# Optimization experiments

Hardware: AMD Instinct MI355X
Metric: run time of the kernel (lower is better)

## Reference

```python
import jax, jax.numpy as jnp
import numpy as np

B, S, H, V = 64, 256, 512, 512


def setup_inputs() -> dict:
    key = jax.random.key(0)
    ks = jax.random.split(key, 13)
    s = 1.0 / np.sqrt(H)
    f = jnp.float32
    return {
        "encoder_outputs": jax.random.normal(ks[0], (B, S, H), f),
        "Wa": jax.random.normal(ks[1], (H, H), f) * s,
        "ba": jax.random.normal(ks[2], (H,), f) * s,
        "Ua": jax.random.normal(ks[3], (H, H), f) * s,
        "bu": jax.random.normal(ks[4], (H,), f) * s,
        "Va": jax.random.normal(ks[5], (1, H), f) * s,
        "bv": jax.random.normal(ks[6], (1,), f) * s,
        "W_ih": jax.random.normal(ks[7], (3 * H, H), f) * s,
        "b_ih": jax.random.normal(ks[8], (3 * H,), f) * s,
        "W_hh": jax.random.normal(ks[9], (3 * H, H), f) * s,
        "b_hh": jax.random.normal(ks[10], (3 * H,), f) * s,
        "Wout": jax.random.normal(ks[11], (V, H), f) * s,
        "bout": jax.random.normal(ks[12], (V,), f) * s,
    }


def reference(encoder_outputs, Wa, ba, Ua, bu, Va, bv,
              W_ih, b_ih, W_hh, b_hh, Wout, bout):
    b, seq_len, h_dim = encoder_outputs.shape
    # Ua(keys) is loop-invariant: precompute once. [B,S,H]
    keys_proj = jnp.einsum('bsh,kh->bsk', encoder_outputs, Ua) + bu
    va = Va[0]  # [H]

    def step(h, _):
        # Bahdanau attention: query = current hidden [B,H]
        q = h @ Wa.T + ba                                   # [B,H]
        e = jnp.tanh(q[:, None, :] + keys_proj)             # [B,S,H]
        scores = jnp.einsum('bsh,h->bs', e, va) + bv[0]     # [B,S]
        w = jax.nn.softmax(scores, axis=-1)                 # [B,S]
        ctx = jnp.einsum('bs,bsh->bh', w, encoder_outputs)  # [B,H]
        # GRU cell (PyTorch gate order: r, z, n)
        gi = ctx @ W_ih.T + b_ih                            # [B,3H]
        gh = h @ W_hh.T + b_hh                              # [B,3H]
        gi_r, gi_z, gi_n = jnp.split(gi, 3, axis=-1)
        gh_r, gh_z, gh_n = jnp.split(gh, 3, axis=-1)
        r = jax.nn.sigmoid(gi_r + gh_r)
        z = jax.nn.sigmoid(gi_z + gh_z)
        n = jnp.tanh(gi_n + r * gh_n)
        h_new = (1.0 - z) * n + z * h                       # [B,H]
        logits = h_new @ Wout.T + bout                      # [B,V]
        return h_new, (logits, w)

    h0 = jnp.zeros((b, h_dim), encoder_outputs.dtype)
    h_final, (logits, ws) = jax.lax.scan(step, h0, None, length=seq_len)
    log_probs = jax.nn.log_softmax(logits, axis=-1)         # [S,B,V]
    attentions = jnp.transpose(ws, (1, 0, 2))               # [B,S,S]
    return log_probs, h_final[None], attentions
```

## Files before the change

### kernel.cpp

```cpp
#include <hip/hip_runtime.h>


typedef short s8v __attribute__((ext_vector_type(8)));
typedef float f4v __attribute__((ext_vector_type(4)));
typedef float f2v __attribute__((ext_vector_type(2)));

#define OFF_BAR   0u
#define OFF_H     2048u
#define OFF_HBF   133120u
#define OFF_Q     198656u
#define OFF_GH    329728u
#define OFF_CTX   722944u
#define OFF_ZP    854016u
#define OFF_WEXP  855040u
#define OFF_WCAT  920576u
#define OFF_WIH   3542016u
#define OFF_UAB   5114880u
#define OFF_KEYS  5639168u
#define OFF_ENC8  22416384u
#define WS_FULL   30804992u
#define MEMSET_BYTES 198656u

#define OUT_LOGITS 0u
#define OUT_HFIN   8388608u
#define OUT_ATTN   8421376u

__device__ __forceinline__ unsigned short f2bf(float f) {
  union { float f; unsigned u; } a; a.f = f;
  unsigned r = a.u + 0x7fffu + ((a.u >> 16) & 1u);
  return (unsigned short)(r >> 16);
}
__device__ __forceinline__ float bfbits2f(unsigned bits) {
  union { unsigned u; float f; } a; a.u = bits; return a.f;
}
__device__ __forceinline__ float bf2f(unsigned short h) { return bfbits2f((unsigned)h << 16); }

__device__ __forceinline__ float cload(const float* p) {
  return __hip_atomic_load(p, __ATOMIC_RELAXED, __HIP_MEMORY_SCOPE_AGENT);
}
__device__ __forceinline__ void cstore(float* p, float v) {
  __hip_atomic_store(p, v, __ATOMIC_RELAXED, __HIP_MEMORY_SCOPE_AGENT);
}
__device__ __forceinline__ unsigned long long cload64(const unsigned long long* p) {
  return __hip_atomic_load(p, __ATOMIC_RELAXED, __HIP_MEMORY_SCOPE_AGENT);
}
__device__ __forceinline__ void cstore64(unsigned long long* p, unsigned long long v) {
  __hip_atomic_store(p, v, __ATOMIC_RELAXED, __HIP_MEMORY_SCOPE_AGENT);
}
__device__ __forceinline__ unsigned long long pack2f(float a, float b) {
  union { float f[2]; unsigned long long u; } x; x.f[0] = a; x.f[1] = b; return x.u;
}

__device__ __forceinline__ float sigm(float x) {
  return __builtin_amdgcn_rcpf(1.f + __expf(-x));
}
__device__ __forceinline__ float tanh2(float x) {
  return 1.f - 2.f * __builtin_amdgcn_rcpf(1.f + __expf(x + x));
}
__device__ __forceinline__ f4v mfma16(s8v a, s8v b, f4v c) {
  return __builtin_amdgcn_mfma_f32_16x16x32_bf16(a, b, c, 0, 0, 0);
}

__device__ __forceinline__ void gbar(unsigned* bar, unsigned& gen) {
  asm volatile("s_waitcnt vmcnt(0) lgkmcnt(0)" ::: "memory");
  __syncthreads();
  if (threadIdx.x == 0) {
    __atomic_signal_fence(__ATOMIC_SEQ_CST);
    gen++;
    const int leaf = blockIdx.x >> 5;
    unsigned old = __hip_atomic_fetch_add(bar + 16 + leaf * 16, 1u, __ATOMIC_RELAXED,
                                          __HIP_MEMORY_SCOPE_AGENT);
    if (old == gen * 32u - 1u) {
      unsigned ro = __hip_atomic_fetch_add(bar, 1u, __ATOMIC_RELAXED,
                                           __HIP_MEMORY_SCOPE_AGENT);
      if (ro == gen * 8u - 1u) {
#pragma unroll
        for (int l = 0; l < 8; ++l)
          __hip_atomic_store(bar + 160 + l * 16, gen, __ATOMIC_RELAXED,
                             __HIP_MEMORY_SCOPE_AGENT);
      }
    }
    while (__hip_atomic_load(bar + 160 + leaf * 16, __ATOMIC_RELAXED,
                             __HIP_MEMORY_SCOPE_AGENT) < gen)
      __builtin_amdgcn_s_sleep(1);
    __atomic_signal_fence(__ATOMIC_SEQ_CST);
  }
  __syncthreads();
}

__global__ void __launch_bounds__(256) prep_kernel(
    const float* __restrict__ Wa, const float* __restrict__ Whh,
    const float* __restrict__ Wout, const float* __restrict__ Wih,
    const float* __restrict__ Ua, const float* __restrict__ enc,
    unsigned short* __restrict__ wcat, unsigned short* __restrict__ wihb,
    unsigned short* __restrict__ uab, unsigned char* __restrict__ enc8,
    int use_enc8) {
  const size_t gid = (size_t)blockIdx.x * 256 + threadIdx.x;
  const size_t stride = (size_t)gridDim.x * 256;
  for (size_t i = gid; i < 2359296u; i += stride) {
    float v; unsigned short* d;
    if (i < 1310720u) {
      v = (i < 262144u) ? Wa[i] : (i < 1048576u) ? Whh[i - 262144u] : Wout[i - 1048576u];
      d = wcat + i;
    } else if (i < 2097152u) { v = Wih[i - 1310720u]; d = wihb + (i - 1310720u); }
    else                     { v = Ua[i - 2097152u];  d = uab  + (i - 2097152u); }
    *d = f2bf(v);
  }
  if (use_enc8) {
    for (size_t j = gid; j < 4194304u; j += stride) {
      float2 e = ((const float2*)enc)[j];
      int pk = __builtin_amdgcn_cvt_pk_fp8_f32(e.x, e.y, 0, false);
      ((unsigned short*)enc8)[j] = (unsigned short)(pk & 0xffff);
    }
  }
}

__global__ void __launch_bounds__(256) keys_kernel(
    const float* __restrict__ enc, const unsigned short* __restrict__ uab,
    const float* __restrict__ bu, unsigned short* __restrict__ keysb) {
  const int tid = threadIdx.x;
  const int w = tid >> 6, lane = tid & 63, ln = lane & 15, kq = lane >> 4;
  const int mb = blockIdx.x >> 3, nb = blockIdx.x & 7;
  const int mrow = mb * 64 + w * 16 + ln;
  f4v acc[4] = {{0,0,0,0},{0,0,0,0},{0,0,0,0},{0,0,0,0}};
  for (int ks = 0; ks < 16; ++ks) {
    const float* ap = enc + (size_t)mrow * 512 + ks * 32 + kq * 8;
    s8v af;
#pragma unroll
    for (int j = 0; j < 8; ++j) af[j] = (short)f2bf(ap[j]);
#pragma unroll
    for (int nt = 0; nt < 4; ++nt) {
      int n = nb * 64 + nt * 16 + ln;
      s8v bf = ((const s8v*)(uab + (size_t)n * 512))[ks * 4 + kq];
      acc[nt] = mfma16(af, bf, acc[nt]);
    }
  }
#pragma unroll
  for (int nt = 0; nt < 4; ++nt) {
    int n = nb * 64 + nt * 16 + ln;
    float bias = bu[n];
#pragma unroll
    for (int r = 0; r < 4; ++r) {
      int gm = mb * 64 + w * 16 + kq * 4 + r;
      keysb[(size_t)gm * 512 + n] = f2bf(__expf(2.f * (acc[nt][r] + bias)));
    }
  }
}

__global__ void __launch_bounds__(256, 1) decoder_kernel(
    const float* __restrict__ enc, const float* __restrict__ ba_,
    const float* __restrict__ va_, const float* __restrict__ bih_,
    const float* __restrict__ bhh_, const float* __restrict__ bout_,
    const unsigned short* __restrict__ wcat, const unsigned short* __restrict__ wih,
    const unsigned short* __restrict__ keysb, const unsigned char* __restrict__ enc8,
    unsigned* __restrict__ bar, float* __restrict__ hst,
    unsigned short* __restrict__ hbf, float* __restrict__ qst,
    float* __restrict__ ghst, float* __restrict__ ctxst,
    float* __restrict__ zpst, float* __restrict__ wexpst,
    float* __restrict__ out, int use_enc8) {
  const int bid = blockIdx.x, tid = threadIdx.x;
  const int w = tid >> 6, lane = tid & 63, ln = lane & 15, kq = lane >> 4;
  __shared__ float s_w[64];
  unsigned gen = 0;
  float* logits = out + OUT_LOGITS;
  float* hfin = out + OUT_HFIN;
  float* attn = out + OUT_ATTN;

  const int pb_b = (bid & 7) * 8 + ((bid >> 3) >> 2);
  const int pb_p = (bid >> 3) & 3;
  float vav[8]; float vasum = 0.f;
#pragma unroll
  for (int j = 0; j < 8; ++j) { vav[j] = va_[lane * 8 + j]; vasum += vav[j]; }
#pragma unroll
  for (int off = 32; off > 0; off >>= 1) vasum += __shfl_xor(vasum, off, 64);

#pragma clang loop unroll(disable)
  for (int it = 0; it <= 256; ++it) {
    if (bid < 160) {
      const int C0 = bid * 16;
      const int rg = (C0 < 512) ? 0 : (C0 < 2048) ? 1 : 2;
      if (!((rg == 2 && it == 0) || (rg != 2 && it == 256))) {
        const s8v* wp = (const s8v*)(wcat + (size_t)(C0 + ln) * 512);
        const unsigned long long* hb =
            (const unsigned long long*)(hbf + (size_t)(w * 16 + ln) * 512);
        unsigned long long t[32];
#pragma unroll
        for (int ks = 0; ks < 16; ++ks) {
          t[2 * ks]     = cload64(hb + ks * 8 + kq * 2);
          t[2 * ks + 1] = cload64(hb + ks * 8 + kq * 2 + 1);
        }
        f4v acc = {0.f, 0.f, 0.f, 0.f};
#pragma unroll
        for (int ks = 0; ks < 16; ++ks) {
          union { unsigned long long u[2]; s8v v; } au;
          au.u[0] = t[2 * ks]; au.u[1] = t[2 * ks + 1];
          acc = mfma16(au.v, wp[ks * 4 + kq], acc);
        }
        const int col = C0 + ln;
        float bias = (rg == 0) ? ba_[col] : (rg == 1) ? bhh_[col - 512] : bout_[col - 2048];
#pragma unroll
        for (int r = 0; r < 4; ++r) {
          int b = w * 16 + kq * 4 + r;
          float v = acc[r] + bias;
          if (rg == 0)      cstore(qst + (size_t)b * 512 + col, v);
          else if (rg == 1) cstore(ghst + (size_t)b * 1536 + (col - 512), v);
          else if (it > 0)
            cstore(logits + (size_t)(it - 1) * 32768 + (size_t)b * 512 + (col - 2048), v);
        }
      }
    } else if (bid < 224 && it < 256) {
      int i = (bid - 160) * 512 + tid;
      cstore(ctxst + i, 0.f);
      cstore(ctxst + i + 256, 0.f);
    }
    gbar(bar, gen);
    if (it == 256) break;

    {
      const unsigned long long* q64 =
          (const unsigned long long*)(qst + (size_t)pb_b * 512 + lane * 8);
      unsigned long long tq[4];
#pragma unroll
      for (int j = 0; j < 4; ++j) tq[j] = cload64(q64 + j);
      union { unsigned long long u[4]; float f[8]; } qu;
#pragma unroll
      for (int j = 0; j < 4; ++j) qu.u[j] = tq[j];
      float Eq[8];
#pragma unroll
      for (int j = 0; j < 8; ++j) Eq[j] = __expf(2.f * qu.f[j]);
#pragma unroll 4
      for (int i = 0; i < 16; ++i) {
        const int sl = w * 16 + i;
        const s8v kv =
            ((const s8v*)(keysb + (size_t)(pb_b * 256 + pb_p * 64 + sl) * 512))[lane];
        float a2 = 0.f;
#pragma unroll
        for (int j = 0; j < 8; ++j) {
          float P = Eq[j] * bf2f((unsigned short)kv[j]);
          a2 += vav[j] * __builtin_amdgcn_rcpf(1.f + P);
        }
#pragma unroll
        for (int off = 32; off > 0; off >>= 1) a2 += __shfl_xor(a2, off, 64);
        if (lane == 0) s_w[sl] = __expf(vasum - 2.f * a2);
      }
      __syncthreads();
      float c0 = 0.f, c1 = 0.f;
      if (use_enc8) {
        const unsigned char* ep = enc8 + (size_t)(pb_b * 256 + pb_p * 64) * 512 + tid * 2;
#pragma unroll 8
        for (int s = 0; s < 64; ++s) {
          float wt = s_w[s];
          unsigned short e8 = *(const unsigned short*)(ep + (size_t)s * 512);
          f2v ef = __builtin_amdgcn_cvt_pk_f32_fp8((int)e8, false);
          c0 += wt * ef[0];
          c1 += wt * ef[1];
        }
      } else {
#pragma unroll 8
        for (int s = 0; s < 64; ++s) {
          float wt = s_w[s];
          float2 e = ((const float2*)(enc + (size_t)(pb_b * 256 + pb_p * 64 + s) * 512))[tid];
          c0 += wt * e.x; c1 += wt * e.y;
        }
      }
      atomicAdd(ctxst + (size_t)pb_b * 512 + tid * 2, c0);
      atomicAdd(ctxst + (size_t)pb_b * 512 + tid * 2 + 1, c1);
      if (tid < 64) {
        float z = s_w[tid];
        cstore(wexpst + (size_t)pb_b * 256 + pb_p * 64 + tid, z);
#pragma unroll
        for (int off = 32; off > 0; off >>= 1) z += __shfl_xor(z, off, 64);
        if (tid == 0) cstore(zpst + pb_b * 4 + pb_p, z);
      }
    }
    gbar(bar, gen);

    if (bid < 32) {
      const int b = w * 16 + ln;
      const unsigned long long* zp64 = (const unsigned long long*)(zpst + b * 4);
      const unsigned long long* cx = (const unsigned long long*)(ctxst + (size_t)b * 512);
      unsigned long long tz0 = cload64(zp64), tz1 = cload64(zp64 + 1);
      unsigned long long t[32];
#pragma unroll
      for (int ks = 0; ks < 8; ++ks)
#pragma unroll
        for (int u = 0; u < 4; ++u)
          t[ks * 4 + u] = cload64(cx + ks * 16 + kq * 4 + u);
      union { unsigned long long u; float f[2]; } z0, z1;
      z0.u = tz0; z1.u = tz1;
      float Z = z0.f[0] + z0.f[1] + z1.f[0] + z1.f[1];
      float invZ = __builtin_amdgcn_rcpf(Z);
      unsigned long long t2[32];
#pragma unroll
      for (int ks = 0; ks < 8; ++ks)
#pragma unroll
        for (int u = 0; u < 4; ++u)
          t2[ks * 4 + u] = cload64(cx + (ks + 8) * 16 + kq * 4 + u);
      f4v ar = {0,0,0,0}, az = {0,0,0,0}, an = {0,0,0,0};
      const s8v* wr = (const s8v*)(wih + (size_t)(bid * 16 + ln) * 512);
      const s8v* wz = (const s8v*)(wih + (size_t)(512 + bid * 16 + ln) * 512);
      const s8v* wn = (const s8v*)(wih + (size_t)(1024 + bid * 16 + ln) * 512);
#pragma unroll
      for (int ks = 0; ks < 16; ++ks) {
        union { unsigned long long u[4]; float f[8]; } cu;
#pragma unroll
        for (int u = 0; u < 4; ++u)
          cu.u[u] = (ks < 8) ? t[ks * 4 + u] : t2[(ks - 8) * 4 + u];
        s8v bfv;
#pragma unroll
        for (int j = 0; j < 8; ++j) bfv[j] = (short)f2bf(cu.f[j] * invZ);
        int idx = ks * 4 + kq;
        ar = mfma16(wr[idx], bfv, ar);
        az = mfma16(wz[idx], bfv, az);
        an = mfma16(wn[idx], bfv, an);
      }
      const int c0i = bid * 16 + kq * 4;
      const int cq = c0i >> 1;
      const unsigned long long* gh64 = (const unsigned long long*)(ghst + (size_t)b * 1536);
      const unsigned long long* h64  = (const unsigned long long*)(hst + (size_t)b * 512);
      unsigned long long tg[8];
      tg[0] = cload64(gh64 + cq);       tg[1] = cload64(gh64 + cq + 1);
      tg[2] = cload64(gh64 + 256 + cq); tg[3] = cload64(gh64 + 256 + cq + 1);
      tg[4] = cload64(gh64 + 512 + cq); tg[5] = cload64(gh64 + 512 + cq + 1);
      tg[6] = cload64(h64 + cq);        tg[7] = cload64(h64 + cq + 1);
      union { unsigned long long u[2]; float f[4]; } gr, gz, gn, hh;
      gr.u[0] = tg[0]; gr.u[1] = tg[1];
      gz.u[0] = tg[2]; gz.u[1] = tg[3];
      gn.u[0] = tg[4]; gn.u[1] = tg[5];
      hh.u[0] = tg[6]; hh.u[1] = tg[7];
      float hn[4]; unsigned short h4[4];
#pragma unroll
      for (int r = 0; r < 4; ++r) {
        int c = c0i + r;
        float rg2 = sigm(ar[r] + bih_[c] + gr.f[r]);
        float zg = sigm(az[r] + bih_[512 + c] + gz.f[r]);
        float ng = tanh2(an[r] + bih_[1024 + c] + rg2 * gn.f[r]);
        hn[r] = (1.f - zg) * ng + zg * hh.f[r];
        h4[r] = f2bf(hn[r]);
      }
      cstore64((unsigned long long*)(hst + (size_t)b * 512 + c0i), pack2f(hn[0], hn[1]));
      cstore64((unsigned long long*)(hst + (size_t)b * 512 + c0i + 2), pack2f(hn[2], hn[3]));
      union { unsigned short s[4]; unsigned long long u; } hb4;
      hb4.s[0] = h4[0]; hb4.s[1] = h4[1]; hb4.s[2] = h4[2]; hb4.s[3] = h4[3];
      cstore64((unsigned long long*)(hbf + (size_t)b * 512 + c0i), hb4.u);
    } else if (bid < 96) {
      const int b = bid - 32;
      unsigned long long tz0 = cload64((const unsigned long long*)(zpst + b * 4));
      unsigned long long tz1 = cload64((const unsigned long long*)(zpst + b * 4) + 1);
      float we = cload(wexpst + (size_t)b * 256 + tid);
      union { unsigned long long u; float f[2]; } z0, z1;
      z0.u = tz0; z1.u = tz1;
      float Z = z0.f[0] + z0.f[1] + z1.f[0] + z1.f[1];
      attn[(size_t)b * 65536 + (size_t)it * 256 + tid] = we * __builtin_amdgcn_rcpf(Z);
    }
    gbar(bar, gen);
  }

  for (int rit = 0; rit < 16; ++rit) {
    int row = bid * 64 + rit * 4 + w;
    float* xr = logits + (size_t)row * 512;
    f4v a = ((const f4v*)xr)[lane * 2];
    f4v b2 = ((const f4v*)xr)[lane * 2 + 1];
    float m = a[0];
#pragma unroll
    for (int j = 1; j < 4; ++j) m = fmaxf(m, a[j]);
#pragma unroll
    for (int j = 0; j < 4; ++j) m = fmaxf(m, b2[j]);
#pragma unroll
    for (int off = 32; off > 0; off >>= 1) m = fmaxf(m, __shfl_xor(m, off, 64));
    float sm = 0.f;
#pragma unroll
    for (int j = 0; j < 4; ++j) sm += __expf(a[j] - m) + __expf(b2[j] - m);
#pragma unroll
    for (int off = 32; off > 0; off >>= 1) sm += __shfl_xor(sm, off, 64);
    float lse = m + __logf(sm);
    f4v oa, ob;
#pragma unroll
    for (int j = 0; j < 4; ++j) { oa[j] = a[j] - lse; ob[j] = b2[j] - lse; }
    ((f4v*)xr)[lane * 2] = oa;
    ((f4v*)xr)[lane * 2 + 1] = ob;
  }
  {
    int i = bid * 256 + tid;
    if (i < 32768) hfin[i] = cload(hst + i);
  }
}

extern "C" void kernel_launch(void* const* d_in, const int* in_sizes, int n_in,
                              void* d_out, int out_size, void* d_ws, size_t ws_size,
                              hipStream_t stream) {
  const float* enc  = (const float*)d_in[0];
  const float* Wa   = (const float*)d_in[1];
  const float* ba   = (const float*)d_in[2];
  const float* Ua   = (const float*)d_in[3];
  const float* bu   = (const float*)d_in[4];
  const float* Va   = (const float*)d_in[5];
  const float* Wih  = (const float*)d_in[7];
  const float* bih  = (const float*)d_in[8];
  const float* Whh  = (const float*)d_in[9];
  const float* bhh  = (const float*)d_in[10];
  const float* Wout = (const float*)d_in[11];
  const float* bout = (const float*)d_in[12];
  (void)in_sizes; (void)n_in; (void)out_size;

  char* ws = (char*)d_ws;
  unsigned*       bar   = (unsigned*)(ws + OFF_BAR);
  float*          hst   = (float*)(ws + OFF_H);
  unsigned short* hbf   = (unsigned short*)(ws + OFF_HBF);
  float*          qst   = (float*)(ws + OFF_Q);
  float*          ghst  = (float*)(ws + OFF_GH);
  float*          ctxst = (float*)(ws + OFF_CTX);
  float*          zpst  = (float*)(ws + OFF_ZP);
  float*          wexp  = (float*)(ws + OFF_WEXP);
  unsigned short* wcat  = (unsigned short*)(ws + OFF_WCAT);
  unsigned short* wihb  = (unsigned short*)(ws + OFF_WIH);
  unsigned short* uab   = (unsigned short*)(ws + OFF_UAB);
  unsigned short* keysb = (unsigned short*)(ws + OFF_KEYS);
  unsigned char*  enc8  = (unsigned char*)(ws + OFF_ENC8);
  int use_enc8 = (ws_size >= (size_t)WS_FULL) ? 1 : 0;

  hipMemsetAsync(d_ws, 0, MEMSET_BYTES, stream);
  prep_kernel<<<1024, 256, 0, stream>>>(Wa, Whh, Wout, Wih, Ua, enc,
                                        wcat, wihb, uab, enc8, use_enc8);
  keys_kernel<<<2048, 256, 0, stream>>>(enc, uab, bu, keysb);
  decoder_kernel<<<256, 256, 0, stream>>>(enc, ba, Va, bih, bhh, bout,
                                          wcat, wihb, keysb, enc8,
                                          bar, hst, hbf, qst, ghst, ctxst,
                                          zpst, wexp, (float*)d_out, use_enc8);
}
```

Baseline: 10.10 ms.

## Restructure decoder into 64 batch-owning blocks with flat barrier and transposed keys

Rewrites the persistent decoder so each of 64 blocks of 512 threads owns one batch row. Attention scores, softmax and the context are computed entirely within that block, using a transposed keys layout and shared-memory reductions, which replaces cross-block atomic context accumulation. The two-level tree barrier becomes a single-counter barrier over 64 blocks. GRU and output projections are redistributed, with the gh and logits partials accumulated in zeroed workspace and output buffers, and the bout bias is folded into the final log-softmax. The output buffer now needs an extra memset. Fewer blocks means less parallelism per step in exchange for fewer global synchronisations and less cross-block traffic.

```diff
diff --git a/kernel.cpp b/kernel.cpp
--- a/kernel.cpp
+++ b/kernel.cpp
@@ -6,20 +6,17 @@
 typedef float f2v __attribute__((ext_vector_type(2)));
 
 #define OFF_BAR   0u
-#define OFF_H     2048u
-#define OFF_HBF   133120u
-#define OFF_Q     198656u
-#define OFF_GH    329728u
-#define OFF_CTX   722944u
-#define OFF_ZP    854016u
-#define OFF_WEXP  855040u
-#define OFF_WCAT  920576u
-#define OFF_WIH   3542016u
-#define OFF_UAB   5114880u
-#define OFF_KEYS  5639168u
-#define OFF_ENC8  22416384u
-#define WS_FULL   30804992u
-#define MEMSET_BYTES 198656u
+#define OFF_Q     4096u
+#define OFF_GH    135168u
+#define OFF_CTX   921600u
+#define OFF_WA    987136u
+#define OFF_WHH   1511424u
+#define OFF_WIH   3084288u
+#define OFF_WOUT  4657152u
+#define OFF_KEYS  5181440u
+#define OFF_ENC8  21958656u
+#define WS_FULL   30347264u
+#define MEMSET_BYTES 921600u
 
 #define OUT_LOGITS 0u
 #define OUT_HFIN   8388608u
@@ -30,27 +27,21 @@
   unsigned r = a.u + 0x7fffu + ((a.u >> 16) & 1u);
   return (unsigned short)(r >> 16);
 }
-__device__ __forceinline__ float bfbits2f(unsigned bits) {
-  union { unsigned u; float f; } a; a.u = bits; return a.f;
-}
-__device__ __forceinline__ float bf2f(unsigned short h) { return bfbits2f((unsigned)h << 16); }
-
+__device__ __forceinline__ float bf2f(unsigned short h) {
+  union { unsigned u; float f; } a; a.u = (unsigned)h << 16; return a.f;
+}
 __device__ __forceinline__ float cload(const float* p) {
   return __hip_atomic_load(p, __ATOMIC_RELAXED, __HIP_MEMORY_SCOPE_AGENT);
 }
 __device__ __forceinline__ void cstore(float* p, float v) {
   __hip_atomic_store(p, v, __ATOMIC_RELAXED, __HIP_MEMORY_SCOPE_AGENT);
 }
+__device__ __forceinline__ void cstoreu(unsigned* p, unsigned v) {
+  __hip_atomic_store(p, v, __ATOMIC_RELAXED, __HIP_MEMORY_SCOPE_AGENT);
+}
 __device__ __forceinline__ unsigned long long cload64(const unsigned long long* p) {
   return __hip_atomic_load(p, __ATOMIC_RELAXED, __HIP_MEMORY_SCOPE_AGENT);
 }
-__device__ __forceinline__ void cstore64(unsigned long long* p, unsigned long long v) {
-  __hip_atomic_store(p, v, __ATOMIC_RELAXED, __HIP_MEMORY_SCOPE_AGENT);
-}
-__device__ __forceinline__ unsigned long long pack2f(float a, float b) {
-  union { float f[2]; unsigned long long u; } x; x.f[0] = a; x.f[1] = b; return x.u;
-}
-
 __device__ __forceinline__ float sigm(float x) {
   return __builtin_amdgcn_rcpf(1.f + __expf(-x));
 }
@@ -67,20 +58,12 @@
   if (threadIdx.x == 0) {
     __atomic_signal_fence(__ATOMIC_SEQ_CST);
     gen++;
-    const int leaf = blockIdx.x >> 5;
-    unsigned old = __hip_atomic_fetch_add(bar + 16 + leaf * 16, 1u, __ATOMIC_RELAXED,
+    unsigned old = __hip_atomic_fetch_add(bar, 1u, __ATOMIC_RELAXED,
                                           __HIP_MEMORY_SCOPE_AGENT);
-    if (old == gen * 32u - 1u) {
-      unsigned ro = __hip_atomic_fetch_add(bar, 1u, __ATOMIC_RELAXED,
-                                           __HIP_MEMORY_SCOPE_AGENT);
-      if (ro == gen * 8u - 1u) {
-#pragma unroll
-        for (int l = 0; l < 8; ++l)
-          __hip_atomic_store(bar + 160 + l * 16, gen, __ATOMIC_RELAXED,
-                             __HIP_MEMORY_SCOPE_AGENT);
-      }
-    }
-    while (__hip_atomic_load(bar + 160 + leaf * 16, __ATOMIC_RELAXED,
+    if (old == gen * 64u - 1u)
+      __hip_atomic_store(bar + 16, gen, __ATOMIC_RELAXED,
+                         __HIP_MEMORY_SCOPE_AGENT);
+    while (__hip_atomic_load(bar + 16, __ATOMIC_RELAXED,
                              __HIP_MEMORY_SCOPE_AGENT) < gen)
       __builtin_amdgcn_s_sleep(1);
     __atomic_signal_fence(__ATOMIC_SEQ_CST);
@@ -90,20 +73,19 @@
 
 __global__ void __launch_bounds__(256) prep_kernel(
     const float* __restrict__ Wa, const float* __restrict__ Whh,
-    const float* __restrict__ Wout, const float* __restrict__ Wih,
-    const float* __restrict__ Ua, const float* __restrict__ enc,
-    unsigned short* __restrict__ wcat, unsigned short* __restrict__ wihb,
-    unsigned short* __restrict__ uab, unsigned char* __restrict__ enc8,
-    int use_enc8) {
+    const float* __restrict__ Wih, const float* __restrict__ Wout,
+    const float* __restrict__ enc,
+    unsigned short* __restrict__ wa_b, unsigned short* __restrict__ whh_b,
+    unsigned short* __restrict__ wih_b, unsigned short* __restrict__ wout_b,
+    unsigned char* __restrict__ enc8, int use_enc8) {
   const size_t gid = (size_t)blockIdx.x * 256 + threadIdx.x;
   const size_t stride = (size_t)gridDim.x * 256;
-  for (size_t i = gid; i < 2359296u; i += stride) {
+  for (size_t i = gid; i < 2097152u; i += stride) {
     float v; unsigned short* d;
-    if (i < 1310720u) {
-      v = (i < 262144u) ? Wa[i] : (i < 1048576u) ? Whh[i - 262144u] : Wout[i - 1048576u];
-      d = wcat + i;
-    } else if (i < 2097152u) { v = Wih[i - 1310720u]; d = wihb + (i - 1310720u); }
-    else                     { v = Ua[i - 2097152u];  d = uab  + (i - 2097152u); }
+    if (i < 262144u)       { v = Wa[i];             d = wa_b + i; }
+    else if (i < 1048576u) { v = Whh[i - 262144u];  d = whh_b + (i - 262144u); }
+    else if (i < 1835008u) { v = Wih[i - 1048576u]; d = wih_b + (i - 1048576u); }
+    else                   { v = Wout[i - 1835008u];d = wout_b + (i - 1835008u); }
     *d = f2bf(v);
   }
   if (use_enc8) {
@@ -116,8 +98,8 @@
 }
 
 __global__ void __launch_bounds__(256) keys_kernel(
-    const float* __restrict__ enc, const unsigned short* __restrict__ uab,
-    const float* __restrict__ bu, unsigned short* __restrict__ keysb) {
+    const float* __restrict__ enc, const float* __restrict__ Ua,
+    const float* __restrict__ bu, unsigned short* __restrict__ keysT) {
   const int tid = threadIdx.x;
   const int w = tid >> 6, lane = tid & 63, ln = lane & 15, kq = lane >> 4;
   const int mb = blockIdx.x >> 3, nb = blockIdx.x & 7;
@@ -131,7 +113,10 @@
 #pragma unroll
     for (int nt = 0; nt < 4; ++nt) {
       int n = nb * 64 + nt * 16 + ln;
-      s8v bf = ((const s8v*)(uab + (size_t)n * 512))[ks * 4 + kq];
+      const float* up = Ua + (size_t)n * 512 + ks * 32 + kq * 8;
+      s8v bf;
+#pragma unroll
+      for (int j = 0; j < 8; ++j) bf[j] = (short)f2bf(up[j]);
       acc[nt] = mfma16(af, bf, acc[nt]);
     }
   }
@@ -142,247 +127,257 @@
 #pragma unroll
     for (int r = 0; r < 4; ++r) {
       int gm = mb * 64 + w * 16 + kq * 4 + r;
-      keysb[(size_t)gm * 512 + n] = f2bf(__expf(2.f * (acc[nt][r] + bias)));
-    }
-  }
-}
-
-__global__ void __launch_bounds__(256, 1) decoder_kernel(
+      int bb = gm >> 8, ss = gm & 255;
+      keysT[(size_t)bb * 131072u + (size_t)n * 256 + ss] =
+          f2bf(__expf(2.f * (acc[nt][r] + bias)));
+    }
+  }
+}
+
+__global__ void __launch_bounds__(512) decoder_kernel(
     const float* __restrict__ enc, const float* __restrict__ ba_,
     const float* __restrict__ va_, const float* __restrict__ bih_,
     const float* __restrict__ bhh_, const float* __restrict__ bout_,
-    const unsigned short* __restrict__ wcat, const unsigned short* __restrict__ wih,
-    const unsigned short* __restrict__ keysb, const unsigned char* __restrict__ enc8,
-    unsigned* __restrict__ bar, float* __restrict__ hst,
-    unsigned short* __restrict__ hbf, float* __restrict__ qst,
-    float* __restrict__ ghst, float* __restrict__ ctxst,
-    float* __restrict__ zpst, float* __restrict__ wexpst,
+    const unsigned short* __restrict__ wa_b, const unsigned short* __restrict__ whh_b,
+    const unsigned short* __restrict__ wih_b, const unsigned short* __restrict__ wout_b,
+    const unsigned short* __restrict__ keysT, const unsigned char* __restrict__ enc8,
+    unsigned* __restrict__ bar, float* __restrict__ qbuf,
+    float* __restrict__ ghsum, unsigned short* __restrict__ ctxg,
     float* __restrict__ out, int use_enc8) {
   const int bid = blockIdx.x, tid = threadIdx.x;
   const int w = tid >> 6, lane = tid & 63, ln = lane & 15, kq = lane >> 4;
-  __shared__ float s_w[64];
+  const int ab = (bid & 7) * 8 + (bid >> 3);
+
+  float* logits = out + OUT_LOGITS;
+  float* hfin   = out + OUT_HFIN;
+  float* attn   = out + OUT_ATTN;
+
+  __shared__ float2 evL[512];
+  __shared__ float swL[256];
+  __shared__ float ZpL[8];
+  __shared__ float cpart[2][256][2];
+  __shared__ float hof[64][65];
+  __shared__ unsigned short hT[64][72];
+
   unsigned gen = 0;
-  float* logits = out + OUT_LOGITS;
-  float* hfin = out + OUT_HFIN;
-  float* attn = out + OUT_ATTN;
-
-  const int pb_b = (bid & 7) * 8 + ((bid >> 3) >> 2);
-  const int pb_p = (bid >> 3) & 3;
-  float vav[8]; float vasum = 0.f;
-#pragma unroll
-  for (int j = 0; j < 8; ++j) { vav[j] = va_[lane * 8 + j]; vasum += vav[j]; }
-#pragma unroll
-  for (int off = 32; off > 0; off >>= 1) vasum += __shfl_xor(vasum, off, 64);
+  const float va_r = va_[tid];
+  const float ba_r = ba_[tid];
+
+  for (int i = tid; i < 64 * 65; i += 512) ((float*)hof)[i] = 0.f;
+  float vs = va_r;
+#pragma unroll
+  for (int off = 32; off > 0; off >>= 1) vs += __shfl_xor(vs, off, 64);
+  if (lane == 0) ZpL[w] = vs;
+  __syncthreads();
+  float vasum = 0.f;
+#pragma unroll
+  for (int l = 0; l < 8; ++l) vasum += ZpL[l];
+  __syncthreads();
+
+  const int m = bid;
+  const int wm = w >> 2, ct = w & 3;
+  const int cl = ct * 16 + ln;
+  float bihv[3] = {0, 0, 0}, bhhv[3] = {0, 0, 0};
+  if (bid < 8) {
+#pragma unroll
+    for (int g = 0; g < 3; ++g) {
+      bihv[g] = bih_[g * 512 + m * 64 + cl];
+      bhhv[g] = bhh_[g * 512 + m * 64 + cl];
+    }
+  }
+  const unsigned short* kb = keysT + (size_t)ab * 131072u;
+  const unsigned char* e8p = enc8 + (size_t)ab * 131072u;
 
 #pragma clang loop unroll(disable)
-  for (int it = 0; it <= 256; ++it) {
-    if (bid < 160) {
-      const int C0 = bid * 16;
-      const int rg = (C0 < 512) ? 0 : (C0 < 2048) ? 1 : 2;
-      if (!((rg == 2 && it == 0) || (rg != 2 && it == 256))) {
-        const s8v* wp = (const s8v*)(wcat + (size_t)(C0 + ln) * 512);
-        const unsigned long long* hb =
-            (const unsigned long long*)(hbf + (size_t)(w * 16 + ln) * 512);
-        unsigned long long t[32];
-#pragma unroll
-        for (int ks = 0; ks < 16; ++ks) {
-          t[2 * ks]     = cload64(hb + ks * 8 + kq * 2);
-          t[2 * ks + 1] = cload64(hb + ks * 8 + kq * 2 + 1);
-        }
-        f4v acc = {0.f, 0.f, 0.f, 0.f};
-#pragma unroll
-        for (int ks = 0; ks < 16; ++ks) {
-          union { unsigned long long u[2]; s8v v; } au;
-          au.u[0] = t[2 * ks]; au.u[1] = t[2 * ks + 1];
-          acc = mfma16(au.v, wp[ks * 4 + kq], acc);
-        }
-        const int col = C0 + ln;
-        float bias = (rg == 0) ? ba_[col] : (rg == 1) ? bhh_[col - 512] : bout_[col - 2048];
-#pragma unroll
-        for (int r = 0; r < 4; ++r) {
-          int b = w * 16 + kq * 4 + r;
-          float v = acc[r] + bias;
-          if (rg == 0)      cstore(qst + (size_t)b * 512 + col, v);
-          else if (rg == 1) cstore(ghst + (size_t)b * 1536 + (col - 512), v);
-          else if (it > 0)
-            cstore(logits + (size_t)(it - 1) * 32768 + (size_t)b * 512 + (col - 2048), v);
-        }
+  for (int t = 0; t < 256; ++t) {
+    {
+      float qv = cload(qbuf + (size_t)ab * 512 + tid);
+      cstore(qbuf + (size_t)ab * 512 + tid, 0.f);
+      float2 ev; ev.x = __expf(2.f * (qv + ba_r)); ev.y = va_r;
+      evL[tid] = ev;
+      float* gz = ghsum + ((t + 1) & 1) * 98304u + bid * 1536;
+      cstore(gz + tid, 0.f); cstore(gz + 512 + tid, 0.f);
+      cstore(gz + 1024 + tid, 0.f);
+    }
+    __syncthreads();
+    {
+      const int s = w * 32 + (lane & 31);
+      const int h0 = (lane >> 5) * 256;
+      const unsigned short* kp = kb + (size_t)h0 * 256 + s;
+      float a2 = 0.f;
+#pragma unroll 8
+      for (int h = 0; h < 256; ++h) {
+        float2 ev = evL[h0 + h];
+        float Ek = bf2f(kp[(size_t)h * 256]);
+        a2 += ev.y * __builtin_amdgcn_rcpf(1.f + ev.x * Ek);
       }
-    } else if (bid < 224 && it < 256) {
-      int i = (bid - 160) * 512 + tid;
-      cstore(ctxst + i, 0.f);
-      cstore(ctxst + i + 256, 0.f);
-    }
-    gbar(bar, gen);
-    if (it == 256) break;
-
+      a2 += __shfl_xor(a2, 32, 64);
+      float wt = __expf(vasum - 2.f * a2);
+      float zp = wt;
+#pragma unroll
+      for (int off = 16; off > 0; off >>= 1) zp += __shfl_xor(zp, off, 64);
+      if (lane < 32) { swL[s] = wt; if (lane == 0) ZpL[w] = zp; }
+    }
+    __syncthreads();
+    float Z = 0.f;
+#pragma unroll
+    for (int l = 0; l < 8; ++l) Z += ZpL[l];
+    float invZ = __builtin_amdgcn_rcpf(Z);
     {
-      const unsigned long long* q64 =
-          (const unsigned long long*)(qst + (size_t)pb_b * 512 + lane * 8);
-      unsigned long long tq[4];
-#pragma unroll
-      for (int j = 0; j < 4; ++j) tq[j] = cload64(q64 + j);
-      union { unsigned long long u[4]; float f[8]; } qu;
-#pragma unroll
-      for (int j = 0; j < 4; ++j) qu.u[j] = tq[j];
-      float Eq[8];
-#pragma unroll
-      for (int j = 0; j < 8; ++j) Eq[j] = __expf(2.f * qu.f[j]);
-#pragma unroll 4
-      for (int i = 0; i < 16; ++i) {
-        const int sl = w * 16 + i;
-        const s8v kv =
-            ((const s8v*)(keysb + (size_t)(pb_b * 256 + pb_p * 64 + sl) * 512))[lane];
-        float a2 = 0.f;
-#pragma unroll
-        for (int j = 0; j < 8; ++j) {
-          float P = Eq[j] * bf2f((unsigned short)kv[j]);
-          a2 += vav[j] * __builtin_amdgcn_rcpf(1.f + P);
-        }
-#pragma unroll
-        for (int off = 32; off > 0; off >>= 1) a2 += __shfl_xor(a2, off, 64);
-        if (lane == 0) s_w[sl] = __expf(vasum - 2.f * a2);
-      }
-      __syncthreads();
+      const int hp = tid & 255, sh = tid >> 8;
+      const int s0 = sh * 128;
       float c0 = 0.f, c1 = 0.f;
       if (use_enc8) {
-        const unsigned char* ep = enc8 + (size_t)(pb_b * 256 + pb_p * 64) * 512 + tid * 2;
+        const unsigned char* ep = e8p + (size_t)s0 * 512 + hp * 2;
 #pragma unroll 8
-        for (int s = 0; s < 64; ++s) {
-          float wt = s_w[s];
-          unsigned short e8 = *(const unsigned short*)(ep + (size_t)s * 512);
-          f2v ef = __builtin_amdgcn_cvt_pk_f32_fp8((int)e8, false);
-          c0 += wt * ef[0];
-          c1 += wt * ef[1];
+        for (int i = 0; i < 128; ++i) {
+          float wt = swL[s0 + i];
+          unsigned short v8 = *(const unsigned short*)(ep + (size_t)i * 512);
+          f2v ef = __builtin_amdgcn_cvt_pk_f32_fp8((int)v8, false);
+          c0 += wt * ef[0]; c1 += wt * ef[1];
         }
       } else {
+        const float2* ep = (const float2*)(enc + (size_t)(ab * 256 + s0) * 512) + hp;
 #pragma unroll 8
-        for (int s = 0; s < 64; ++s) {
-          float wt = s_w[s];
-          float2 e = ((const float2*)(enc + (size_t)(pb_b * 256 + pb_p * 64 + s) * 512))[tid];
+        for (int i = 0; i < 128; ++i) {
+          float wt = swL[s0 + i];
+          float2 e = ep[(size_t)i * 256];
           c0 += wt * e.x; c1 += wt * e.y;
         }
       }
-      atomicAdd(ctxst + (size_t)pb_b * 512 + tid * 2, c0);
-      atomicAdd(ctxst + (size_t)pb_b * 512 + tid * 2 + 1, c1);
-      if (tid < 64) {
-        float z = s_w[tid];
-        cstore(wexpst + (size_t)pb_b * 256 + pb_p * 64 + tid, z);
-#pragma unroll
-        for (int off = 32; off > 0; off >>= 1) z += __shfl_xor(z, off, 64);
-        if (tid == 0) cstore(zpst + pb_b * 4 + pb_p, z);
+      cpart[sh][hp][0] = c0; cpart[sh][hp][1] = c1;
+    }
+    __syncthreads();
+    if (tid < 256) {
+      float cc0 = (cpart[0][tid][0] + cpart[1][tid][0]) * invZ;
+      float cc1 = (cpart[0][tid][1] + cpart[1][tid][1]) * invZ;
+      unsigned pk = (unsigned)f2bf(cc0) | ((unsigned)f2bf(cc1) << 16);
+      cstoreu((unsigned*)ctxg + (size_t)ab * 256 + tid, pk);
+      attn[(size_t)ab * 65536 + (size_t)t * 256 + tid] = swL[tid] * invZ;
+    }
+    gbar(bar, gen);
+
+    if (bid < 8) {
+      const float* ghp = ghsum + (t & 1) * 98304u;
+      float ghv[3][2][4];
+#pragma unroll
+      for (int g = 0; g < 3; ++g)
+#pragma unroll
+        for (int mi = 0; mi < 2; ++mi)
+#pragma unroll
+          for (int r = 0; r < 4; ++r) {
+            int bb = (2 * wm + mi) * 16 + kq * 4 + r;
+            ghv[g][mi][r] = cload(ghp + (size_t)bb * 1536 + g * 512 + m * 64 + cl);
+          }
+      f4v acc[3][2];
+#pragma unroll
+      for (int g = 0; g < 3; ++g)
+#pragma unroll
+        for (int mi = 0; mi < 2; ++mi) acc[g][mi] = (f4v){0.f, 0.f, 0.f, 0.f};
+      const unsigned long long* ca0 =
+          (const unsigned long long*)ctxg + (size_t)(2 * wm * 16 + ln) * 128;
+      const unsigned long long* ca1 = ca0 + 2048;
+      const s8v* wB[3];
+#pragma unroll
+      for (int g = 0; g < 3; ++g)
+        wB[g] = (const s8v*)(wih_b + (size_t)(g * 512 + m * 64 + cl) * 512);
+#pragma unroll 4
+      for (int kt = 0; kt < 16; ++kt) {
+        union { unsigned long long u[2]; s8v v; } a0u, a1u;
+        a0u.u[0] = cload64(ca0 + kt * 8 + kq * 2);
+        a0u.u[1] = cload64(ca0 + kt * 8 + kq * 2 + 1);
+        a1u.u[0] = cload64(ca1 + kt * 8 + kq * 2);
+        a1u.u[1] = cload64(ca1 + kt * 8 + kq * 2 + 1);
+#pragma unroll
+        for (int g = 0; g < 3; ++g) {
+          s8v bf = wB[g][kt * 4 + kq];
+          acc[g][0] = mfma16(a0u.v, bf, acc[g][0]);
+          acc[g][1] = mfma16(a1u.v, bf, acc[g][1]);
+        }
       }
+#pragma unroll
+      for (int mi = 0; mi < 2; ++mi)
+#pragma unroll
+        for (int r = 0; r < 4; ++r) {
+          int bb = (2 * wm + mi) * 16 + kq * 4 + r;
+          float rr = sigm(acc[0][mi][r] + bihv[0] + ghv[0][mi][r] + bhhv[0]);
+          float zz = sigm(acc[1][mi][r] + bihv[1] + ghv[1][mi][r] + bhhv[1]);
+          float nn = tanh2(acc[2][mi][r] + bihv[2] + rr * (ghv[2][mi][r] + bhhv[2]));
+          float ho = hof[bb][cl];
+          float hn = (1.f - zz) * nn + zz * ho;
+          hof[bb][cl] = hn;
+          hT[bb][cl] = f2bf(hn);
+          if (t == 255) hfin[(size_t)bb * 512 + m * 64 + cl] = hn;
+        }
+      __syncthreads();
+      s8v af[2][4];
+#pragma unroll
+      for (int mt = 0; mt < 4; ++mt)
+#pragma unroll
+        for (int k2 = 0; k2 < 2; ++k2)
+          af[k2][mt] = *(const s8v*)&hT[mt * 16 + ln][k2 * 32 + kq * 8];
+      float* ghn = ghsum + ((t + 1) & 1) * 98304u;
+#pragma clang loop unroll(disable)
+      for (int i = 0; i < 20; ++i) {
+        int nt = w + i * 8;
+        const unsigned short* wsrc; float* dst; int rs;
+        if (nt < 32)       { int col = nt * 16 + ln;
+          wsrc = wa_b + (size_t)col * 512; dst = qbuf + col; rs = 512; }
+        else if (nt < 128) { int col = (nt - 32) * 16 + ln;
+          wsrc = whh_b + (size_t)col * 512; dst = ghn + col; rs = 1536; }
+        else               { int col = (nt - 128) * 16 + ln;
+          wsrc = wout_b + (size_t)col * 512;
+          dst = logits + (size_t)t * 32768 + col; rs = 512; }
+        s8v b0 = ((const s8v*)wsrc)[m * 8 + kq];
+        s8v b1 = ((const s8v*)wsrc)[m * 8 + 4 + kq];
+#pragma unroll
+        for (int mt = 0; mt < 4; ++mt) {
+          f4v a4 = {0.f, 0.f, 0.f, 0.f};
+          a4 = mfma16(af[0][mt], b0, a4);
+          a4 = mfma16(af[1][mt], b1, a4);
+#pragma unroll
+          for (int r = 0; r < 4; ++r)
+            atomicAdd(dst + (size_t)(mt * 16 + kq * 4 + r) * rs, a4[r]);
+        }
+      }
     }
     gbar(bar, gen);
-
-    if (bid < 32) {
-      const int b = w * 16 + ln;
-      const unsigned long long* zp64 = (const unsigned long long*)(zpst + b * 4);
-      const unsigned long long* cx = (const unsigned long long*)(ctxst + (size_t)b * 512);
-      unsigned long long tz0 = cload64(zp64), tz1 = cload64(zp64 + 1);
-      unsigned long long t[32];
-#pragma unroll
-      for (int ks = 0; ks < 8; ++ks)
-#pragma unroll
-        for (int u = 0; u < 4; ++u)
-          t[ks * 4 + u] = cload64(cx + ks * 16 + kq * 4 + u);
-      union { unsigned long long u; float f[2]; } z0, z1;
-      z0.u = tz0; z1.u = tz1;
-      float Z = z0.f[0] + z0.f[1] + z1.f[0] + z1.f[1];
-      float invZ = __builtin_amdgcn_rcpf(Z);
-      unsigned long long t2[32];
-#pragma unroll
-      for (int ks = 0; ks < 8; ++ks)
-#pragma unroll
-        for (int u = 0; u < 4; ++u)
-          t2[ks * 4 + u] = cload64(cx + (ks + 8) * 16 + kq * 4 + u);
-      f4v ar = {0,0,0,0}, az = {0,0,0,0}, an = {0,0,0,0};
-      const s8v* wr = (const s8v*)(wih + (size_t)(bid * 16 + ln) * 512);
-      const s8v* wz = (const s8v*)(wih + (size_t)(512 + bid * 16 + ln) * 512);
-      const s8v* wn = (const s8v*)(wih + (size_t)(1024 + bid * 16 + ln) * 512);
-#pragma unroll
-      for (int ks = 0; ks < 16; ++ks) {
-        union { unsigned long long u[4]; float f[8]; } cu;
-#pragma unroll
-        for (int u = 0; u < 4; ++u)
-          cu.u[u] = (ks < 8) ? t[ks * 4 + u] : t2[(ks - 8) * 4 + u];
-        s8v bfv;
-#pragma unroll
-        for (int j = 0; j < 8; ++j) bfv[j] = (short)f2bf(cu.f[j] * invZ);
-        int idx = ks * 4 + kq;
-        ar = mfma16(wr[idx], bfv, ar);
-        az = mfma16(wz[idx], bfv, az);
-        an = mfma16(wn[idx], bfv, an);
-      }
-      const int c0i = bid * 16 + kq * 4;
-      const int cq = c0i >> 1;
-      const unsigned long long* gh64 = (const unsigned long long*)(ghst + (size_t)b * 1536);
-      const unsigned long long* h64  = (const unsigned long long*)(hst + (size_t)b * 512);
-      unsigned long long tg[8];
-      tg[0] = cload64(gh64 + cq);       tg[1] = cload64(gh64 + cq + 1);
-      tg[2] = cload64(gh64 + 256 + cq); tg[3] = cload64(gh64 + 256 + cq + 1);
-      tg[4] = cload64(gh64 + 512 + cq); tg[5] = cload64(gh64 + 512 + cq + 1);
-      tg[6] = cload64(h64 + cq);        tg[7] = cload64(h64 + cq + 1);
-      union { unsigned long long u[2]; float f[4]; } gr, gz, gn, hh;
-      gr.u[0] = tg[0]; gr.u[1] = tg[1];
-      gz.u[0] = tg[2]; gz.u[1] = tg[3];
-      gn.u[0] = tg[4]; gn.u[1] = tg[5];
-      hh.u[0] = tg[6]; hh.u[1] = tg[7];
-      float hn[4]; unsigned short h4[4];
-#pragma unroll
-      for (int r = 0; r < 4; ++r) {
-        int c = c0i + r;
-        float rg2 = sigm(ar[r] + bih_[c] + gr.f[r]);
-        float zg = sigm(az[r] + bih_[512 + c] + gz.f[r]);
-        float ng = tanh2(an[r] + bih_[1024 + c] + rg2 * gn.f[r]);
-        hn[r] = (1.f - zg) * ng + zg * hh.f[r];
-        h4[r] = f2bf(hn[r]);
-      }
-      cstore64((unsigned long long*)(hst + (size_t)b * 512 + c0i), pack2f(hn[0], hn[1]));
-      cstore64((unsigned long long*)(hst + (size_t)b * 512 + c0i + 2), pack2f(hn[2], hn[3]));
-      union { unsigned short s[4]; unsigned long long u; } hb4;
-      hb4.s[0] = h4[0]; hb4.s[1] = h4[1]; hb4.s[2] = h4[2]; hb4.s[3] = h4[3];
-      cstore64((unsigned long long*)(hbf + (size_t)b * 512 + c0i), hb4.u);
-    } else if (bid < 96) {
-      const int b = bid - 32;
-      unsigned long long tz0 = cload64((const unsigned long long*)(zpst + b * 4));
-      unsigned long long tz1 = cload64((const unsigned long long*)(zpst + b * 4) + 1);
-      float we = cload(wexpst + (size_t)b * 256 + tid);
-      union { unsigned long long u; float f[2]; } z0, z1;
-      z0.u = tz0; z1.u = tz1;
-      float Z = z0.f[0] + z0.f[1] + z1.f[0] + z1.f[1];
-      attn[(size_t)b * 65536 + (size_t)it * 256 + tid] = we * __builtin_amdgcn_rcpf(Z);
-    }
-    gbar(bar, gen);
-  }
-
-  for (int rit = 0; rit < 16; ++rit) {
-    int row = bid * 64 + rit * 4 + w;
-    float* xr = logits + (size_t)row * 512;
-    f4v a = ((const f4v*)xr)[lane * 2];
-    f4v b2 = ((const f4v*)xr)[lane * 2 + 1];
-    float m = a[0];
-#pragma unroll
-    for (int j = 1; j < 4; ++j) m = fmaxf(m, a[j]);
-#pragma unroll
-    for (int j = 0; j < 4; ++j) m = fmaxf(m, b2[j]);
-#pragma unroll
-    for (int off = 32; off > 0; off >>= 1) m = fmaxf(m, __shfl_xor(m, off, 64));
+  }
+
+  float bo[8];
+#pragma unroll
+  for (int j = 0; j < 8; ++j) bo[j] = bout_[lane * 8 + j];
+#pragma clang loop unroll(disable)
+  for (int i = 0; i < 32; ++i) {
+    int row = bid * 256 + w * 32 + i;
+    const unsigned long long* xr64 =
+        (const unsigned long long*)(logits + (size_t)row * 512) + lane * 4;
+    unsigned long long t4[4];
+#pragma unroll
+    for (int j = 0; j < 4; ++j) t4[j] = cload64(xr64 + j);
+    union { unsigned long long u[4]; float f[8]; } xu;
+#pragma unroll
+    for (int j = 0; j < 4; ++j) xu.u[j] = t4[j];
+    float x[8];
+#pragma unroll
+    for (int j = 0; j < 8; ++j) x[j] = xu.f[j] + bo[j];
+    float mx = x[0];
+#pragma unroll
+    for (int j = 1; j < 8; ++j) mx = fmaxf(mx, x[j]);
+#pragma unroll
+    for (int off = 32; off > 0; off >>= 1) mx = fmaxf(mx, __shfl_xor(mx, off, 64));
     float sm = 0.f;
 #pragma unroll
-    for (int j = 0; j < 4; ++j) sm += __expf(a[j] - m) + __expf(b2[j] - m);
+    for (int j = 0; j < 8; ++j) sm += __expf(x[j] - mx);
 #pragma unroll
     for (int off = 32; off > 0; off >>= 1) sm += __shfl_xor(sm, off, 64);
-    float lse = m + __logf(sm);
-    f4v oa, ob;
-#pragma unroll
-    for (int j = 0; j < 4; ++j) { oa[j] = a[j] - lse; ob[j] = b2[j] - lse; }
-    ((f4v*)xr)[lane * 2] = oa;
-    ((f4v*)xr)[lane * 2 + 1] = ob;
-  }
-  {
-    int i = bid * 256 + tid;
-    if (i < 32768) hfin[i] = cload(hst + i);
+    float lse = mx + __logf(sm);
+    float* xw = logits + (size_t)row * 512 + lane * 8;
+    f4v o0, o1;
+#pragma unroll
+    for (int j = 0; j < 4; ++j) { o0[j] = x[j] - lse; o1[j] = x[4 + j] - lse; }
+    ((f4v*)xw)[0] = o0;
+    ((f4v*)xw)[1] = o1;
   }
 }
 
@@ -404,27 +399,26 @@
   (void)in_sizes; (void)n_in; (void)out_size;
 
   char* ws = (char*)d_ws;
-  unsigned*       bar   = (unsigned*)(ws + OFF_BAR);
-  float*          hst   = (float*)(ws + OFF_H);
-  unsigned short* hbf   = (unsigned short*)(ws + OFF_HBF);
-  float*          qst   = (float*)(ws + OFF_Q);
-  float*          ghst  = (float*)(ws + OFF_GH);
-  float*          ctxst = (float*)(ws + OFF_CTX);
-  float*          zpst  = (float*)(ws + OFF_ZP);
-  float*          wexp  = (float*)(ws + OFF_WEXP);
-  unsigned short* wcat  = (unsigned short*)(ws + OFF_WCAT);
-  unsigned short* wihb  = (unsigned short*)(ws + OFF_WIH);
-  unsigned short* uab   = (unsigned short*)(ws + OFF_UAB);
-  unsigned short* keysb = (unsigned short*)(ws + OFF_KEYS);
-  unsigned char*  enc8  = (unsigned char*)(ws + OFF_ENC8);
+  unsigned*       bar    = (unsigned*)(ws + OFF_BAR);
+  float*          qbuf   = (float*)(ws + OFF_Q);
+  float*          ghsum  = (float*)(ws + OFF_GH);
+  unsigned short* ctxg   = (unsigned short*)(ws + OFF_CTX);
+  unsigned short* wa_b   = (unsigned short*)(ws + OFF_WA);
+  unsigned short* whh_b  = (unsigned short*)(ws + OFF_WHH);
+  unsigned short* wih_b  = (unsigned short*)(ws + OFF_WIH);
+  unsigned short* wout_b = (unsigned short*)(ws + OFF_WOUT);
+  unsigned short* keysT  = (unsigned short*)(ws + OFF_KEYS);
+  unsigned char*  enc8   = (unsigned char*)(ws + OFF_ENC8);
   int use_enc8 = (ws_size >= (size_t)WS_FULL) ? 1 : 0;
 
   hipMemsetAsync(d_ws, 0, MEMSET_BYTES, stream);
-  prep_kernel<<<1024, 256, 0, stream>>>(Wa, Whh, Wout, Wih, Ua, enc,
-                                        wcat, wihb, uab, enc8, use_enc8);
-  keys_kernel<<<2048, 256, 0, stream>>>(enc, uab, bu, keysb);
-  decoder_kernel<<<256, 256, 0, stream>>>(enc, ba, Va, bih, bhh, bout,
-                                          wcat, wihb, keysb, enc8,
-                                          bar, hst, hbf, qst, ghst, ctxst,
-                                          zpst, wexp, (float*)d_out, use_enc8);
-}
+  hipMemsetAsync(d_out, 0, 33554432u, stream);
+  prep_kernel<<<1024, 256, 0, stream>>>(Wa, Whh, Wih, Wout, enc,
+                                        wa_b, whh_b, wih_b, wout_b,
+                                        enc8, use_enc8);
+  keys_kernel<<<2048, 256, 0, stream>>>(enc, Ua, bu, keysT);
+  decoder_kernel<<<64, 512, 0, stream>>>(enc, ba, Va, bih, bhh, bout,
+                                         wa_b, whh_b, wih_b, wout_b,
+                                         keysT, enc8, bar, qbuf, ghsum, ctxg,
+                                         (float*)d_out, use_enc8);
+}
```

Result: slower. 19.04 ms (+88.5%).
